# Optimization experiments

Hardware: AMD Instinct MI355X
Metric: run time of the kernel (lower is better)

## Reference

```python
import jax, jax.numpy as jnp
import numpy as np
import math

NH = 12  # num_attention_heads (multiple of 4 required by pattern dispatch)


def _forward(Input, hidden_states, attention_mask, Wq, bq, Wk, bk, Wv, bv, Wo, bo, L):
    b, n, _, H = Input.shape
    hd = H // NH
    G = NH // 4  # heads per criss-cross pattern
    # boolean-mask gather of valid (head, tail) entity pairs, row-major like torch
    bi, ri, ci = jnp.nonzero(attention_mask > 0, size=L)
    x = Input[bi, ri, ci]            # [L, H] keys/values source
    xq = hidden_states[bi, ri, ci]   # [L, H] query source
    q = (xq @ Wq + bq).reshape(L, NH, hd)
    k = (x @ Wk + bk).reshape(L, NH, hd)
    v = (x @ Wv + bv).reshape(L, NH, hd)
    ar = jnp.arange(n)
    # per-pattern criss-cross masks for query position (b, r, c), each [L, n]
    m0 = attention_mask[bi, ri, :] * (ar[None, :] != ci[:, None])  # row r, exclude self col c
    m1 = attention_mask[bi, :, ci] * (ar[None, :] != ri[:, None])  # col c, exclude self row r
    m2 = attention_mask[bi, :, ri]                                  # col r (no self exclusion)
    m3 = attention_mask[bi, ci, :]                                  # row c (no self exclusion)
    adds = jnp.stack([(1.0 - m) * -10000.0 for m in (m0, m1, m2, m3)], axis=1)  # [L, 4, n]
    # scatter per-pattern head groups into zero grid, then criss-cross gather
    k_gs, v_gs = [], []
    for p in range(4):
        sk = jnp.zeros((b, n, n, G, hd), k.dtype).at[bi, ri, ci].set(k[:, p::4])
        sv = jnp.zeros((b, n, n, G, hd), v.dtype).at[bi, ri, ci].set(v[:, p::4])
        if p == 0:
            gk, gv = sk[bi, ri], sv[bi, ri]          # element [l,k] = grid[b, r, k]
        elif p == 1:
            gk, gv = sk[bi, :, ci], sv[bi, :, ci]    # grid[b, k, c]
        elif p == 2:
            gk, gv = sk[bi, :, ri], sv[bi, :, ri]    # grid[b, k, r]
        else:
            gk, gv = sk[bi, ci], sv[bi, ci]          # grid[b, c, k]
        k_gs.append(gk)
        v_gs.append(gv)
    kg = jnp.stack(k_gs, axis=1)  # [L, 4, n, G, hd]
    vg = jnp.stack(v_gs, axis=1)
    # head h = 4*g + p (k[:, p::4] picks heads p, p+4, p+8)
    kg = kg.transpose(0, 3, 1, 2, 4).reshape(L, NH, n, hd)
    vg = vg.transpose(0, 3, 1, 2, 4).reshape(L, NH, n, hd)
    amask = jnp.broadcast_to(adds[:, None, :, :], (L, G, 4, n)).reshape(L, NH, n)
    # prepend self key/value; NOTE: original code uses additive bias +1.0 (ones) for the self slot
    kf = jnp.concatenate([k[:, :, None, :], kg], axis=2)   # [L, NH, n+1, hd]
    vf = jnp.concatenate([v[:, :, None, :], vg], axis=2)
    amask = jnp.concatenate([jnp.ones((L, NH, 1), amask.dtype), amask], axis=-1)
    scores = jnp.einsum('lhd,lhkd->lhk', q, kf) / math.sqrt(hd) + amask
    probs = jax.nn.softmax(scores, axis=-1)  # dropout is identity in eval
    ctx = jnp.einsum('lhk,lhkd->lhd', probs, vf).reshape(L, H)
    return ctx @ Wo + bo


def setup_inputs() -> dict:
    key = jax.random.key(0)
    ks = jax.random.split(key, 8)
    b, n, H = 2, 40, 768
    Input = jax.random.normal(ks[0], (b, n, n, H), jnp.float32)
    hidden_states = jax.random.normal(ks[1], (b, n, n, H), jnp.float32)
    # all valid entity pairs except self pairs -> deterministic L
    attention_mask = (jnp.ones((b, n, n)) - jnp.eye(n)[None]).astype(jnp.float32)
    L = int(b * n * (n - 1))  # 3120
    std = 0.02
    Wq = std * jax.random.normal(ks[2], (H, H), jnp.float32)
    Wk = std * jax.random.normal(ks[3], (H, H), jnp.float32)
    Wv = std * jax.random.normal(ks[4], (H, H), jnp.float32)
    Wo = std * jax.random.normal(ks[5], (H, H), jnp.float32)
    bq = jnp.zeros((H,), jnp.float32)
    bk = jnp.zeros((H,), jnp.float32)
    bv = jnp.zeros((H,), jnp.float32)
    bo = jnp.zeros((H,), jnp.float32)
    return {"Input": Input, "hidden_states": hidden_states, "attention_mask": attention_mask,
            "Wq": Wq, "bq": bq, "Wk": Wk, "bk": bk, "Wv": Wv, "bv": bv, "Wo": Wo, "bo": bo, "L": L}


def reference(Input, hidden_states, attention_mask, Wq, bq, Wk, bk, Wv, bv, Wo, bo, L):
    return _forward(Input, hidden_states, attention_mask, Wq, bq, Wk, bk, Wv, bv, Wo, bo, L)
```

## Files before the change

kernel.cpp:

```cpp
#include <hip/hip_runtime.h>
#include <hip/hip_bf16.h>
#include <math.h>

#define NHEADS 12

typedef __attribute__((ext_vector_type(4))) float f32x4;
typedef __attribute__((ext_vector_type(8))) short bf16x8;

__device__ __forceinline__ unsigned short f2bf(float x) {
  __hip_bfloat16 h = __float2bfloat16(x);
  return *reinterpret_cast<unsigned short*>(&h);
}
__device__ __forceinline__ float bf2f(unsigned short u) {
  union { unsigned int i; float f; } c; c.i = ((unsigned int)u) << 16; return c.f;
}

__device__ __forceinline__ int xcd_swz(int orig, int nwg) {
  int q = nwg >> 3, r = nwg & 7;
  int xcd = orig & 7, idx = orig >> 3;
  return (xcd < r ? xcd * (q + 1) : r * (q + 1) + (xcd - r) * q) + idx;
}

__global__ __launch_bounds__(256) void prep(const float* __restrict__ mask, int total,
                                            int* __restrict__ pos2l, int* __restrict__ lidx,
                                            const float* __restrict__ bk, const float* __restrict__ bv,
                                            float* __restrict__ bkv,
                                            const float* __restrict__ W0, const float* __restrict__ W1,
                                            const float* __restrict__ W2, const float* __restrict__ W3,
                                            unsigned short* __restrict__ T0, unsigned short* __restrict__ T1,
                                            unsigned short* __restrict__ T2, unsigned short* __restrict__ T3,
                                            const float* __restrict__ hidden, const float* __restrict__ input,
                                            unsigned short* __restrict__ Hbf, unsigned short* __restrict__ Ibf,
                                            int H) {
  int nt32 = H / 32;
  int nw = nt32 * nt32 * 4;
  int bx = blockIdx.x;
  int t = threadIdx.x;
  if (bx < nw) {
    __shared__ float tile[32][33];
    int z = bx / (nt32 * nt32);
    int rem = bx - z * nt32 * nt32;
    int byy = rem / nt32;
    int bxx = rem - byy * nt32;
    const float* W = (z == 0) ? W0 : (z == 1) ? W1 : (z == 2) ? W2 : W3;
    unsigned short* T = (z == 0) ? T0 : (z == 1) ? T1 : (z == 2) ? T2 : T3;
    int k0 = byy * 32, n0 = bxx * 32;
    int kk = t >> 3, n4 = (t & 7) * 4;
    float4 v = *reinterpret_cast<const float4*>(W + (size_t)(k0 + kk) * H + n0 + n4);
    tile[n4 + 0][kk] = v.x; tile[n4 + 1][kk] = v.y; tile[n4 + 2][kk] = v.z; tile[n4 + 3][kk] = v.w;
    __syncthreads();
    int nn2 = t >> 3, k4 = (t & 7) * 4;
#pragma unroll
    for (int e = 0; e < 4; ++e)
      T[(size_t)(n0 + nn2) * H + k0 + k4 + e] = f2bf(tile[nn2][k4 + e]);
  } else if (bx == nw) {
    __shared__ int cnt[256];
    for (int i = t; i < H; i += 256) { bkv[i] = bk[i]; bkv[H + i] = bv[i]; }
    int per = (total + 255) >> 8;
    int begin = t * per;
    int end = begin + per; if (end > total) end = total;
    if (begin > total) begin = total;
    int c = 0;
    for (int i = begin; i < end; ++i) c += (mask[i] > 0.f) ? 1 : 0;
    cnt[t] = c;
    __syncthreads();
    for (int off = 1; off < 256; off <<= 1) {
      int vv = (t >= off) ? cnt[t - off] : 0;
      __syncthreads();
      cnt[t] += vv;
      __syncthreads();
    }
    int excl = cnt[t] - c;
    for (int i = begin; i < end; ++i) {
      if (mask[i] > 0.f) { pos2l[i] = excl; lidx[excl] = i; ++excl; }
      else pos2l[i] = -1;
    }
  } else {
    int idx = bx - nw - 1;
    int perarr = (total * H) >> 11;
    int which = idx / perarr;
    size_t off = (size_t)(idx - which * perarr) * 2048 + t * 8;
    const float* src = which ? input : hidden;
    unsigned short* dst = which ? Ibf : Hbf;
    float4 a = *reinterpret_cast<const float4*>(src + off);
    float4 b2 = *reinterpret_cast<const float4*>(src + off + 4);
    bf16x8 st;
    st[0]=f2bf(a.x); st[1]=f2bf(a.y); st[2]=f2bf(a.z); st[3]=f2bf(a.w);
    st[4]=f2bf(b2.x); st[5]=f2bf(b2.y); st[6]=f2bf(b2.z); st[7]=f2bf(b2.w);
    *reinterpret_cast<bf16x8*>(dst + off) = st;
  }
}

#define QBM 128
#define QBN 128
#define QBK 64

template <bool OUT_BF16, bool GATHER>
__device__ __forceinline__ void gemm128_core(const unsigned short* __restrict__ A,
                                             const int* __restrict__ lidx,
                                             const unsigned short* __restrict__ Bt,
                                             const float* __restrict__ bias,
                                             void* __restrict__ C,
                                             int M, int N, int K, int m0, int n0,
                                             unsigned short* sA, unsigned short* sB) {
  int tid = threadIdx.x;
  int wid = tid >> 6, lane = tid & 63;
  int wm = wid >> 1, wn = wid & 1;
  int lr = lane & 15, lq = lane >> 4;
  f32x4 acc[4][4] = {};

  const unsigned short* aptr[4];
  const unsigned short* bptr[4];
#pragma unroll
  for (int r = 0; r < 4; ++r) {
    int c = (r * 4 + wid) * 64 + lane;
    int row = c >> 3, sl = c & 7;
    int sg = sl ^ (row & 7);
    int gm = m0 + row; if (gm >= M) gm = M - 1;
    size_t abase = GATHER ? (size_t)lidx[gm] * K : (size_t)gm * K;
    aptr[r] = A + abase + sg * 8;
    bptr[r] = Bt + (size_t)(n0 + row) * K + sg * 8;
  }

  for (int k0 = 0; k0 < K; k0 += QBK) {
#pragma unroll
    for (int r = 0; r < 4; ++r)
      __builtin_amdgcn_global_load_lds((const __attribute__((address_space(1))) unsigned int*)(aptr[r] + k0),
                                       (__attribute__((address_space(3))) unsigned int*)(sA + (r * 4 + wid) * 512),
                                       16, 0, 0);
#pragma unroll
    for (int r = 0; r < 4; ++r)
      __builtin_amdgcn_global_load_lds((const __attribute__((address_space(1))) unsigned int*)(bptr[r] + k0),
                                       (__attribute__((address_space(3))) unsigned int*)(sB + (r * 4 + wid) * 512),
                                       16, 0, 0);
    __syncthreads();
#pragma unroll
    for (int ks = 0; ks < 2; ++ks) {
      bf16x8 af[4], bfr[4];
#pragma unroll
      for (int i = 0; i < 4; ++i) {
        int row = wm * 64 + i * 16 + lr;
        int slot = (ks * 4 + lq) ^ (row & 7);
        af[i] = *reinterpret_cast<const bf16x8*>(sA + row * 64 + slot * 8);
      }
#pragma unroll
      for (int j = 0; j < 4; ++j) {
        int rn = wn * 64 + j * 16 + lr;
        int slot = (ks * 4 + lq) ^ (rn & 7);
        bfr[j] = *reinterpret_cast<const bf16x8*>(sB + rn * 64 + slot * 8);
      }
#pragma unroll
      for (int i = 0; i < 4; ++i)
#pragma unroll
        for (int j = 0; j < 4; ++j)
          acc[i][j] = __builtin_amdgcn_mfma_f32_16x16x32_bf16(af[i], bfr[j], acc[i][j], 0, 0, 0);
    }
    __syncthreads();
  }

#pragma unroll
  for (int i = 0; i < 4; ++i) {
#pragma unroll
    for (int j = 0; j < 4; ++j) {
      int gcol = n0 + wn * 64 + j * 16 + lr;
      float bv = bias[gcol];
      int rbase = m0 + wm * 64 + i * 16 + lq * 4;
#pragma unroll
      for (int r = 0; r < 4; ++r) {
        int gm = rbase + r;
        if (gm >= M) continue;
        float val = acc[i][j][r] + bv;
        if (OUT_BF16) ((unsigned short*)C)[(size_t)gm * N + gcol] = f2bf(val);
        else          ((float*)C)[(size_t)gm * N + gcol] = val;
      }
    }
  }
}

__global__ __launch_bounds__(256) void gemm_qkv(const unsigned short* __restrict__ Hbf,
                                                const unsigned short* __restrict__ Ibf,
                                                const unsigned short* __restrict__ Wqt,
                                                const unsigned short* __restrict__ Wkvt,
                                                const float* __restrict__ bq,
                                                const float* __restrict__ bkv,
                                                const int* __restrict__ lidx,
                                                unsigned short* __restrict__ Cq,
                                                unsigned short* __restrict__ Ckv,
                                                int M, int K, int H, int NX) {
  __shared__ unsigned short sA[QBM * QBK];
  __shared__ unsigned short sB[QBN * QBK];
  int wgid = xcd_swz(blockIdx.x, gridDim.x);
  int y = wgid / NX, x = wgid - y * NX;
  int m0 = y * QBM;
  int nq = H / QBN;
  if (x < nq)
    gemm128_core<true, true>(Hbf, lidx, Wqt, bq, Cq, M, H, K, m0, x * QBN, sA, sB);
  else
    gemm128_core<true, true>(Ibf, lidx, Wkvt, bkv, Ckv, M, 2 * H, K, m0, (x - nq) * QBN, sA, sB);
}

#define GBM 128
#define GBN 64
#define GBK 64

__global__ __launch_bounds__(256) void gemm_out(const unsigned short* __restrict__ A,
                                                const unsigned short* __restrict__ Bt,
                                                const float* __restrict__ bias,
                                                float* __restrict__ C,
                                                int M, int N, int K) {
  __shared__ unsigned short sA[GBM * GBK];
  __shared__ unsigned short sB[GBN * GBK];
  int NX = N / GBN;
  int wgid = xcd_swz(blockIdx.x, gridDim.x);
  int y = wgid / NX, x = wgid - y * NX;
  int m0 = y * GBM, n0 = x * GBN;
  int tid = threadIdx.x;
  int wid = tid >> 6, lane = tid & 63;
  int wm = wid >> 1, wn = wid & 1;
  int lr = lane & 15, lq = lane >> 4;
  f32x4 acc[4][2] = {};

  const unsigned short* aptr[4];
  const unsigned short* bptr[2];
#pragma unroll
  for (int r = 0; r < 4; ++r) {
    int c = (r * 4 + wid) * 64 + lane;
    int row = c >> 3, sl = c & 7;
    int sg = sl ^ (row & 7);
    aptr[r] = A + (size_t)(m0 + row) * K + sg * 8;
    if (r < 2) bptr[r] = Bt + (size_t)(n0 + row) * K + sg * 8;
  }

  for (int k0 = 0; k0 < K; k0 += GBK) {
#pragma unroll
    for (int r = 0; r < 4; ++r)
      __builtin_amdgcn_global_load_lds((const __attribute__((address_space(1))) unsigned int*)(aptr[r] + k0),
                                       (__attribute__((address_space(3))) unsigned int*)(sA + (r * 4 + wid) * 512),
                                       16, 0, 0);
#pragma unroll
    for (int r = 0; r < 2; ++r)
      __builtin_amdgcn_global_load_lds((const __attribute__((address_space(1))) unsigned int*)(bptr[r] + k0),
                                       (__attribute__((address_space(3))) unsigned int*)(sB + (r * 4 + wid) * 512),
                                       16, 0, 0);
    __syncthreads();
#pragma unroll
    for (int ks = 0; ks < 2; ++ks) {
      bf16x8 af[4], bfr[2];
#pragma unroll
      for (int i = 0; i < 4; ++i) {
        int row = wm * 64 + i * 16 + lr;
        int slot = (ks * 4 + lq) ^ (row & 7);
        af[i] = *reinterpret_cast<const bf16x8*>(sA + row * 64 + slot * 8);
      }
#pragma unroll
      for (int j = 0; j < 2; ++j) {
        int rn = wn * 32 + j * 16 + lr;
        int slot = (ks * 4 + lq) ^ (rn & 7);
        bfr[j] = *reinterpret_cast<const bf16x8*>(sB + rn * 64 + slot * 8);
      }
#pragma unroll
      for (int i = 0; i < 4; ++i)
#pragma unroll
        for (int j = 0; j < 2; ++j)
          acc[i][j] = __builtin_amdgcn_mfma_f32_16x16x32_bf16(af[i], bfr[j], acc[i][j], 0, 0, 0);
    }
    __syncthreads();
  }

#pragma unroll
  for (int i = 0; i < 4; ++i) {
#pragma unroll
    for (int j = 0; j < 2; ++j) {
      int gcol = n0 + wn * 32 + j * 16 + lr;
      float bv = bias[gcol];
      int rbase = m0 + wm * 64 + i * 16 + lq * 4;
#pragma unroll
      for (int r = 0; r < 4; ++r) {
        int gm = rbase + r;
        if (gm >= M) continue;
        C[(size_t)gm * N + gcol] = acc[i][j][r] + bv;
      }
    }
  }
}

__global__ __launch_bounds__(128) void attn3(const unsigned short* __restrict__ qb,
                                             const unsigned short* __restrict__ KVb,
                                             const float* __restrict__ mask,
                                             const int* __restrict__ pos2l,
                                             unsigned short* __restrict__ ctx,
                                             int n, int H) {
  __shared__ unsigned short Ks[40 * 72];
  __shared__ unsigned short Vs[40 * 72];
  __shared__ float S[40][42];
  __shared__ float mrow[40];
  __shared__ int qlist[40];

  int bx = blockIdx.x;
  int r0 = bx % n;
  int h3 = (bx / n) % 3;
  int p = (bx / (3 * n)) % 4;
  int bi = bx / (12 * n);
  int h = p + 4 * h3;
  int nn = n * n;
  bool rowkeys = (p == 0 || p == 3);
  bool rowq = (p == 0 || p == 2);
  bool excl = (p < 2);
  int t = threadIdx.x;
  int H2 = 2 * H;

  if (t < 80) {
    int half = t / 40, j = t % 40;
    int keypos = rowkeys ? (r0 * n + j) : (j * n + r0);
    int l2 = pos2l[bi * nn + keypos];
    unsigned short* dst = (half ? Vs : Ks) + j * 72;
    if (l2 >= 0) {
      const unsigned short* src = KVb + (size_t)l2 * H2 + half * H + h * 64;
#pragma unroll
      for (int e8 = 0; e8 < 8; ++e8)
        *reinterpret_cast<bf16x8*>(dst + e8 * 8) = *reinterpret_cast<const bf16x8*>(src + e8 * 8);
    } else {
      bf16x8 z = {};
#pragma unroll
      for (int e8 = 0; e8 < 8; ++e8) *reinterpret_cast<bf16x8*>(dst + e8 * 8) = z;
    }
  }
  if (t < 40) {
    mrow[t] = rowkeys ? mask[bi * nn + r0 * n + t] : mask[bi * nn + t * n + r0];
    int qpos = rowq ? (r0 * n + t) : (t * n + r0);
    qlist[t] = pos2l[bi * nn + qpos];
  }
  __syncthreads();

  int c = t % 40;
  int role = t / 40;
  int lq = (t < 80) ? qlist[c] : -1;

  if (lq >= 0) {
    float qf[64];
    const unsigned short* qp = qb + (size_t)lq * H + h * 64;
#pragma unroll
    for (int e8 = 0; e8 < 8; ++e8) {
      bf16x8 t8 = *reinterpret_cast<const bf16x8*>(qp + e8 * 8);
#pragma unroll
      for (int e = 0; e < 8; ++e) qf[e8 * 8 + e] = bf2f((unsigned short)t8[e]);
    }
    int j0 = role * 20;
#pragma unroll 2
    for (int j = j0; j < j0 + 20; ++j) {
      float acc = 0.f;
#pragma unroll
      for (int e8 = 0; e8 < 8; ++e8) {
        bf16x8 kv = *reinterpret_cast<const bf16x8*>(Ks + j * 72 + e8 * 8);
#pragma unroll
        for (int e = 0; e < 8; ++e) acc = fmaf(qf[e8 * 8 + e], bf2f((unsigned short)kv[e]), acc);
      }
      float mval = mrow[j] * ((excl && j == c) ? 0.f : 1.f);
      S[c][j] = acc * 0.125f + (1.f - mval) * -10000.f;
    }
    if (role == 0) {
      const unsigned short* kp = KVb + (size_t)lq * H2 + h * 64;
      float acc = 0.f;
#pragma unroll
      for (int e8 = 0; e8 < 8; ++e8) {
        bf16x8 kv = *reinterpret_cast<const bf16x8*>(kp + e8 * 8);
#pragma unroll
        for (int e = 0; e < 8; ++e) acc = fmaf(qf[e8 * 8 + e], bf2f((unsigned short)kv[e]), acc);
      }
      S[c][40] = acc * 0.125f + 1.0f;
    }
  }
  __syncthreads();

  if (t < 40 && qlist[t] >= 0) {
    float mx = -3.0e38f;
    for (int j = 0; j <= 40; ++j) mx = fmaxf(mx, S[t][j]);
    float sum = 0.f;
    for (int j = 0; j <= 40; ++j) { float e = __expf(S[t][j] - mx); S[t][j] = e; sum += e; }
    float inv = 1.f / sum;
    for (int j = 0; j <= 40; ++j) S[t][j] *= inv;
  }
  __syncthreads();

  if (lq >= 0) {
    int d0 = role * 32;
    const unsigned short* vsp = KVb + (size_t)lq * H2 + H + h * 64 + d0;
    float pself = S[c][40];
#pragma unroll
    for (int ch = 0; ch < 4; ++ch) {
      int dd = d0 + ch * 8;
      float facc[8];
      bf16x8 vself = *reinterpret_cast<const bf16x8*>(vsp + ch * 8);
#pragma unroll
      for (int e = 0; e < 8; ++e) facc[e] = pself * bf2f((unsigned short)vself[e]);
      for (int j = 0; j < 40; ++j) {
        float pj = S[c][j];
        bf16x8 vv = *reinterpret_cast<const bf16x8*>(Vs + j * 72 + dd);
#pragma unroll
        for (int e = 0; e < 8; ++e) facc[e] = fmaf(pj, bf2f((unsigned short)vv[e]), facc[e]);
      }
      bf16x8 st;
#pragma unroll
      for (int e = 0; e < 8; ++e) st[e] = f2bf(facc[e]);
      *reinterpret_cast<bf16x8*>(ctx + (size_t)lq * H + h * 64 + dd) = st;
    }
  }
}

extern "C" void kernel_launch(void* const* d_in, const int* in_sizes, int n_in,
                              void* d_out, int out_size, void* d_ws, size_t ws_size,
                              hipStream_t stream) {
  const float* Input  = (const float*)d_in[0];
  const float* hidden = (const float*)d_in[1];
  const float* mask   = (const float*)d_in[2];
  const float* Wq = (const float*)d_in[3];
  const float* bq = (const float*)d_in[4];
  const float* Wk = (const float*)d_in[5];
  const float* bk = (const float*)d_in[6];
  const float* Wv = (const float*)d_in[7];
  const float* bv = (const float*)d_in[8];
  const float* Wo = (const float*)d_in[9];
  const float* bo = (const float*)d_in[10];

  int H = (int)llround(sqrt((double)in_sizes[3]));
  int total = in_sizes[2];
  int L = out_size / H;
  int bn = total - L;
  int n = total / bn;
  int b = bn / n;
  int mtiles = (L + QBM - 1) / QBM;
  int Mpad = mtiles * QBM;
  size_t aElems = (size_t)Mpad * H;
  size_t posElems = (size_t)total * H;

  char* p = (char*)d_ws;
  auto take = [&](size_t bytes) { char* r = p; p += (bytes + 255) & ~(size_t)255; return r; };
  int* lidx  = (int*)take((size_t)L * 4);
  int* pos2l = (int*)take((size_t)total * 4);
  float* bkv = (float*)take((size_t)2 * H * 4);
  unsigned short* Wqt  = (unsigned short*)take((size_t)H * H * 2);
  unsigned short* Wot  = (unsigned short*)take((size_t)H * H * 2);
  unsigned short* Wkvt = (unsigned short*)take((size_t)2 * H * H * 2);
  unsigned short* Hbf  = (unsigned short*)take(posElems * 2);
  unsigned short* Ibf  = (unsigned short*)take(posElems * 2);
  unsigned short* qb2  = (unsigned short*)take(aElems * 2);
  unsigned short* KVb  = (unsigned short*)take(aElems * 2 * 2);
  unsigned short* ctxb = (unsigned short*)take(aElems * 2);

  int nt32 = H / 32;
  int nwconv = nt32 * nt32 * 4;
  int nconv = 2 * (int)((posElems) >> 11);
  prep<<<nwconv + 1 + nconv, 256, 0, stream>>>(mask, total, pos2l, lidx, bk, bv, bkv,
                                               Wq, Wk, Wv, Wo,
                                               Wqt, Wkvt, Wkvt + (size_t)H * H, Wot,
                                               hidden, Input, Hbf, Ibf, H);
  {
    int NX = 3 * H / QBN;
    gemm_qkv<<<NX * mtiles, 256, 0, stream>>>(Hbf, Ibf, Wqt, Wkvt, bq, bkv, lidx,
                                              qb2, KVb, L, H, H, NX);
  }
  attn3<<<b * 4 * 3 * n, 128, 0, stream>>>(qb2, KVb, mask, pos2l, ctxb, n, H);
  gemm_out<<<(H / GBN) * mtiles, 256, 0, stream>>>(ctxb, Wot, bo, (float*)d_out, L, H, H);
}
```

Measured before the change: 86.10 us.

## Double-buffer LDS tiles in QKV and output GEMMs to overlap loads with MFMA

Both the fused QKV GEMM and the output-projection GEMM now keep two LDS buffers per operand. The next K tile is issued with global_load_lds while the current one is consumed by MFMAs, and a partial vmcnt wait covers only the older tile. This is meant to hide global-memory latency behind compute. LDS use doubles, which may lower occupancy, and the hand-written vmcnt counts must match the number of loads issued per stage.

```diff
diff --git a/kernel.cpp b/kernel.cpp
--- a/kernel.cpp
+++ b/kernel.cpp
@@ -122,18 +122,33 @@
     bptr[r] = Bt + (size_t)(n0 + row) * K + sg * 8;
   }
 
-  for (int k0 = 0; k0 < K; k0 += QBK) {
+  auto STAGE = [&](int buf, int k0) {
 #pragma unroll
     for (int r = 0; r < 4; ++r)
       __builtin_amdgcn_global_load_lds((const __attribute__((address_space(1))) unsigned int*)(aptr[r] + k0),
-                                       (__attribute__((address_space(3))) unsigned int*)(sA + (r * 4 + wid) * 512),
+                                       (__attribute__((address_space(3))) unsigned int*)(sA + buf * (QBM * QBK) + (r * 4 + wid) * 512),
                                        16, 0, 0);
 #pragma unroll
     for (int r = 0; r < 4; ++r)
       __builtin_amdgcn_global_load_lds((const __attribute__((address_space(1))) unsigned int*)(bptr[r] + k0),
-                                       (__attribute__((address_space(3))) unsigned int*)(sB + (r * 4 + wid) * 512),
+                                       (__attribute__((address_space(3))) unsigned int*)(sB + buf * (QBN * QBK) + (r * 4 + wid) * 512),
                                        16, 0, 0);
-    __syncthreads();
+  };
+
+  const int nt = K / QBK;
+  STAGE(0, 0);
+  int cur = 0;
+  for (int t = 0; t < nt; ++t) {
+    if (t + 1 < nt) {
+      STAGE(cur ^ 1, (t + 1) * QBK);
+      asm volatile("s_waitcnt vmcnt(8)" ::: "memory");
+    } else {
+      asm volatile("s_waitcnt vmcnt(0)" ::: "memory");
+    }
+    __builtin_amdgcn_s_barrier();
+    __builtin_amdgcn_sched_barrier(0);
+    const unsigned short* pA = sA + cur * (QBM * QBK);
+    const unsigned short* pB = sB + cur * (QBN * QBK);
 #pragma unroll
     for (int ks = 0; ks < 2; ++ks) {
       bf16x8 af[4], bfr[4];
@@ -141,13 +156,13 @@
       for (int i = 0; i < 4; ++i) {
         int row = wm * 64 + i * 16 + lr;
         int slot = (ks * 4 + lq) ^ (row & 7);
-        af[i] = *reinterpret_cast<const bf16x8*>(sA + row * 64 + slot * 8);
+        af[i] = *reinterpret_cast<const bf16x8*>(pA + row * 64 + slot * 8);
       }
 #pragma unroll
       for (int j = 0; j < 4; ++j) {
         int rn = wn * 64 + j * 16 + lr;
         int slot = (ks * 4 + lq) ^ (rn & 7);
-        bfr[j] = *reinterpret_cast<const bf16x8*>(sB + rn * 64 + slot * 8);
+        bfr[j] = *reinterpret_cast<const bf16x8*>(pB + rn * 64 + slot * 8);
       }
 #pragma unroll
       for (int i = 0; i < 4; ++i)
@@ -155,7 +170,9 @@
         for (int j = 0; j < 4; ++j)
           acc[i][j] = __builtin_amdgcn_mfma_f32_16x16x32_bf16(af[i], bfr[j], acc[i][j], 0, 0, 0);
     }
-    __syncthreads();
+    __builtin_amdgcn_sched_barrier(0);
+    __builtin_amdgcn_s_barrier();
+    cur ^= 1;
   }
 
 #pragma unroll
@@ -187,8 +204,8 @@
                                                 unsigned short* __restrict__ Cq,
                                                 unsigned short* __restrict__ Ckv,
                                                 int M, int K, int H, int NX) {
-  __shared__ unsigned short sA[QBM * QBK];
-  __shared__ unsigned short sB[QBN * QBK];
+  __shared__ unsigned short sA[2 * QBM * QBK];
+  __shared__ unsigned short sB[2 * QBN * QBK];
   int wgid = xcd_swz(blockIdx.x, gridDim.x);
   int y = wgid / NX, x = wgid - y * NX;
   int m0 = y * QBM;
@@ -208,8 +225,8 @@
                                                 const float* __restrict__ bias,
                                                 float* __restrict__ C,
                                                 int M, int N, int K) {
-  __shared__ unsigned short sA[GBM * GBK];
-  __shared__ unsigned short sB[GBN * GBK];
+  __shared__ unsigned short sA[2 * GBM * GBK];
+  __shared__ unsigned short sB[2 * GBN * GBK];
   int NX = N / GBN;
   int wgid = xcd_swz(blockIdx.x, gridDim.x);
   int y = wgid / NX, x = wgid - y * NX;
@@ -231,18 +248,33 @@
     if (r < 2) bptr[r] = Bt + (size_t)(n0 + row) * K + sg * 8;
   }
 
-  for (int k0 = 0; k0 < K; k0 += GBK) {
+  auto STAGE = [&](int buf, int k0) {
 #pragma unroll
     for (int r = 0; r < 4; ++r)
       __builtin_amdgcn_global_load_lds((const __attribute__((address_space(1))) unsigned int*)(aptr[r] + k0),
-                                       (__attribute__((address_space(3))) unsigned int*)(sA + (r * 4 + wid) * 512),
+                                       (__attribute__((address_space(3))) unsigned int*)(sA + buf * (GBM * GBK) + (r * 4 + wid) * 512),
                                        16, 0, 0);
 #pragma unroll
     for (int r = 0; r < 2; ++r)
       __builtin_amdgcn_global_load_lds((const __attribute__((address_space(1))) unsigned int*)(bptr[r] + k0),
-                                       (__attribute__((address_space(3))) unsigned int*)(sB + (r * 4 + wid) * 512),
+                                       (__attribute__((address_space(3))) unsigned int*)(sB + buf * (GBN * GBK) + (r * 4 + wid) * 512),
                                        16, 0, 0);
-    __syncthreads();
+  };
+
+  const int nt = K / GBK;
+  STAGE(0, 0);
+  int cur = 0;
+  for (int t = 0; t < nt; ++t) {
+    if (t + 1 < nt) {
+      STAGE(cur ^ 1, (t + 1) * GBK);
+      asm volatile("s_waitcnt vmcnt(6)" ::: "memory");
+    } else {
+      asm volatile("s_waitcnt vmcnt(0)" ::: "memory");
+    }
+    __builtin_amdgcn_s_barrier();
+    __builtin_amdgcn_sched_barrier(0);
+    const unsigned short* pA = sA + cur * (GBM * GBK);
+    const unsigned short* pB = sB + cur * (GBN * GBK);
 #pragma unroll
     for (int ks = 0; ks < 2; ++ks) {
       bf16x8 af[4], bfr[2];
@@ -250,13 +282,13 @@
       for (int i = 0; i < 4; ++i) {
         int row = wm * 64 + i * 16 + lr;
         int slot = (ks * 4 + lq) ^ (row & 7);
-        af[i] = *reinterpret_cast<const bf16x8*>(sA + row * 64 + slot * 8);
+        af[i] = *reinterpret_cast<const bf16x8*>(pA + row * 64 + slot * 8);
       }
 #pragma unroll
       for (int j = 0; j < 2; ++j) {
         int rn = wn * 32 + j * 16 + lr;
         int slot = (ks * 4 + lq) ^ (rn & 7);
-        bfr[j] = *reinterpret_cast<const bf16x8*>(sB + rn * 64 + slot * 8);
+        bfr[j] = *reinterpret_cast<const bf16x8*>(pB + rn * 64 + slot * 8);
       }
 #pragma unroll
       for (int i = 0; i < 4; ++i)
@@ -264,7 +296,9 @@
         for (int j = 0; j < 2; ++j)
           acc[i][j] = __builtin_amdgcn_mfma_f32_16x16x32_bf16(af[i], bfr[j], acc[i][j], 0, 0, 0);
     }
-    __syncthreads();
+    __builtin_amdgcn_sched_barrier(0);
+    __builtin_amdgcn_s_barrier();
+    cur ^= 1;
   }
 
 #pragma unroll
```

Result: no change. 86.51 us (+0.5%).
